# Kernel tuning notes

Measured on AMD Instinct MI355X. Metric: run time of the kernel, lower is better.

## Reference

```python
import jax, jax.numpy as jnp
import numpy as np

N_NODE = 8192
H1 = 512
R_EMB = 128
N_EDGE = 262144
N_REG = 2048


def gcn_conv(x, W, b, src, dst, n):
    """PyG-style GCNConv: add self-loops, sym-normalize, linear, scatter-add."""
    h = x @ W  # [n, out]
    loop = jnp.arange(n)
    src2 = jnp.concatenate([src, loop])
    dst2 = jnp.concatenate([dst, loop])
    ones = jnp.ones(src2.shape[0], dtype=h.dtype)
    deg = jax.ops.segment_sum(ones, dst2, num_segments=n)  # in-degree incl. self-loop
    dis = jnp.where(deg > 0, jax.lax.rsqrt(deg), 0.0)
    norm = dis[src2] * dis[dst2]  # [E+n]
    msg = h[src2] * norm[:, None]  # gather + scale
    return jax.ops.segment_sum(msg, dst2, num_segments=n) + b


def setup_inputs() -> dict:
    key = jax.random.key(0)
    k1, k2, k3, k4 = jax.random.split(key, 4)
    edge_index = jax.random.randint(k1, (N_EDGE, 2), 0, N_NODE)  # [E,2] (src,dst) pairs
    reg_id = jax.random.randint(k2, (N_REG,), 0, N_NODE)
    W1 = jax.random.normal(k3, (N_NODE, H1), dtype=jnp.float32) * 0.02
    b1 = jnp.zeros((H1,), dtype=jnp.float32)
    W2 = jax.random.normal(k4, (H1, R_EMB), dtype=jnp.float32) * 0.02
    b2 = jnp.zeros((R_EMB,), dtype=jnp.float32)
    return {"reg_id": reg_id, "edge_index": edge_index, "W1": W1, "b1": b1, "W2": W2, "b2": b2}


def reference(reg_id, edge_index, W1, b1, W2, b2):
    src = edge_index[:, 0]
    dst = edge_index[:, 1]
    n = W1.shape[0]
    x = jnp.eye(n, dtype=W1.dtype)  # identity feature matrix (one-hot per node)
    h = jax.nn.relu(gcn_conv(x, W1, b1, src, dst, n))
    # dropout is identity at inference
    out = gcn_conv(h, W2, b2, src, dst, n)  # [n, R_EMB]
    return out[reg_id]
```

## Files before the change

### kernel.cpp

```cpp
#include <hip/hip_runtime.h>
#include <hip/hip_bf16.h>

typedef unsigned int u32;

#define N_NODE 8192
#define H1 512
#define R_EMB 128
#define N_EDGE 262144
#define N_REG 2048

#define OFF_DEG        (0)
#define OFF_ROWSTART   (64 * 1024)
#define OFF_CURSOR     (128 * 1024)
#define OFF_DIS        (160 * 1024)
#define OFF_SORTED     (256 * 1024)
#define OFF_W1H        (2 * 1024 * 1024)
#define OFF_H1H        (10 * 1024 * 1024)
#define OFF_W2T        (18 * 1024 * 1024)
#define OFF_G          (19 * 1024 * 1024)

#define HALF_U32 (N_NODE * 128)

__device__ inline u32 rne_bf16(float f) {
    u32 u = __float_as_uint(f);
    u += 0x7fffu + ((u >> 16) & 1u);
    return u >> 16;
}
__device__ inline float bf_lo(u32 u) { return __uint_as_float(u << 16); }
__device__ inline float bf_hi(u32 u) { return __uint_as_float(u & 0xffff0000u); }

using frag_ab = __attribute__((ext_vector_type(8))) short;
using frag_cd = __attribute__((ext_vector_type(4))) float;

#define ACC4(v, q) \
    v##0 += bf_lo(q.x); v##1 += bf_hi(q.x); \
    v##2 += bf_lo(q.y); v##3 += bf_hi(q.y);

__global__ void hist_kernel(const int* __restrict__ edge, int* __restrict__ deg) {
    int e = blockIdx.x * blockDim.x + threadIdx.x;
    if (e < N_EDGE) {
        int dst = edge[2 * e + 1];
        atomicAdd(&deg[dst], 1);
    }
}

__global__ void scan_kernel(const int* __restrict__ deg, int* __restrict__ row_start,
                            int* __restrict__ cursor, float* __restrict__ dis) {
    __shared__ int wtot[16];
    __shared__ int wpre[16];
    int t = threadIdx.x;
    int lane = t & 63;
    int wv = t >> 6;
    int base = t * 8;
    int local[8];
    int sum = 0;
#pragma unroll
    for (int j = 0; j < 8; j++) {
        local[j] = deg[base + j];
        sum += local[j];
    }
    int sc = sum;
#pragma unroll
    for (int off = 1; off < 64; off <<= 1) {
        int y = __shfl_up(sc, off, 64);
        if (lane >= off) sc += y;
    }
    if (lane == 63) wtot[wv] = sc;
    __syncthreads();
    if (wv == 0 && lane < 16) {
        int v = wtot[lane];
        int s2 = v;
#pragma unroll
        for (int off = 1; off < 16; off <<= 1) {
            int y = __shfl_up(s2, off, 64);
            if (lane >= off) s2 += y;
        }
        wpre[lane] = s2 - v;
    }
    __syncthreads();
    int run = wpre[wv] + (sc - sum);
#pragma unroll
    for (int j = 0; j < 8; j++) {
        row_start[base + j] = run;
        cursor[base + j] = run;
        dis[base + j] = rsqrtf((float)(local[j] + 1));
        run += local[j];
    }
    if (t == 1023) row_start[N_NODE] = run;
}

__global__ void prep_kernel(const int* __restrict__ edge, int* __restrict__ cursor,
                            int* __restrict__ sorted_src,
                            const float* __restrict__ W1, const float* __restrict__ dis,
                            u32* __restrict__ W1h,
                            const float* __restrict__ W2, u32* __restrict__ w2t) {
    int bid = blockIdx.x;
    if (bid < 1024) {
        int e = bid * 256 + threadIdx.x;
        int src = edge[2 * e + 0];
        int dst = edge[2 * e + 1];
        int pos = atomicAdd(&cursor[dst], 1);
        sorted_src[pos] = src;
    } else if (bid < 5120) {
        int idx = (bid - 1024) * 256 + threadIdx.x;
        int j2 = idx & 63;
        int row = (idx >> 6) & 8191;
        int h = idx >> 19;
        float d = dis[row];
        float4 f = *(const float4*)(W1 + ((size_t)row << 9) + (h << 8) + (j2 << 2));
        uint2 o;
        o.x = rne_bf16(f.x * d) | (rne_bf16(f.y * d) << 16);
        o.y = rne_bf16(f.z * d) | (rne_bf16(f.w * d) << 16);
        *(uint2*)(W1h + ((size_t)h * HALF_U32) + (row << 7) + (j2 << 1)) = o;
    } else {
        int idx = (bid - 5120) * 256 + threadIdx.x;
        int j = idx >> 8;
        int p = idx & 255;
        float a = W2[(size_t)(2 * p) * R_EMB + j];
        float b = W2[(size_t)(2 * p + 1) * R_EMB + j];
        w2t[idx] = rne_bf16(a) | (rne_bf16(b) << 16);
    }
}

__global__ __launch_bounds__(256) void layer1_half(const u32* __restrict__ W1h,
                                                   const float* __restrict__ b1,
                                                   const int* __restrict__ row_start,
                                                   const int* __restrict__ sorted_src,
                                                   const float* __restrict__ dis,
                                                   u32* __restrict__ h1h) {
    int half = blockIdx.x >> 11;
    int d = ((blockIdx.x & 2047) << 2) + (threadIdx.x >> 6);
    int lane = threadIdx.x & 63;
    const u32* basep = W1h + (size_t)half * HALF_U32;
    int loff = lane << 1;
    float disd = dis[d];

    uint2 wd = *(const uint2*)(basep + (d << 7) + loff);
    float a0 = bf_lo(wd.x), a1 = bf_hi(wd.x), a2 = bf_lo(wd.y), a3 = bf_hi(wd.y);
    float c0 = 0, c1 = 0, c2 = 0, c3 = 0;

    int beg = row_start[d], end = row_start[d + 1];
    int i = beg;
    int rem = (end - beg) & 3;
    for (int r = 0; r < rem; r++) {
        int s = sorted_src[i++];
        uint2 v0 = *(const uint2*)(basep + (s << 7) + loff);
        ACC4(a, v0)
    }
    for (; i < end; i += 4) {
        int s0 = sorted_src[i];
        int s1 = sorted_src[i + 1];
        int s2 = sorted_src[i + 2];
        int s3 = sorted_src[i + 3];
        uint2 v0 = *(const uint2*)(basep + (s0 << 7) + loff);
        uint2 v1 = *(const uint2*)(basep + (s1 << 7) + loff);
        uint2 v2 = *(const uint2*)(basep + (s2 << 7) + loff);
        uint2 v3 = *(const uint2*)(basep + (s3 << 7) + loff);
        ACC4(a, v0)
        ACC4(c, v1)
        ACC4(a, v2)
        ACC4(c, v3)
    }
    a0 += c0; a1 += c1; a2 += c2; a3 += c3;

    float4 bb = *(const float4*)(b1 + (half << 8) + (lane << 2));
    float o0 = fmaxf(a0 * disd + bb.x, 0.0f) * disd;
    float o1 = fmaxf(a1 * disd + bb.y, 0.0f) * disd;
    float o2 = fmaxf(a2 * disd + bb.z, 0.0f) * disd;
    float o3 = fmaxf(a3 * disd + bb.w, 0.0f) * disd;
    uint2 o;
    o.x = rne_bf16(o0) | (rne_bf16(o1) << 16);
    o.y = rne_bf16(o2) | (rne_bf16(o3) << 16);
    *(uint2*)(h1h + (size_t)half * HALF_U32 + (d << 7) + loff) = o;
}

__global__ __launch_bounds__(256) void layer2_agg(const u32* __restrict__ h1h,
                                                  const int* __restrict__ reg_id,
                                                  const int* __restrict__ row_start,
                                                  const int* __restrict__ sorted_src,
                                                  const float* __restrict__ dis,
                                                  u32* __restrict__ g_bf) {
    int tgt = (blockIdx.x << 2) + (threadIdx.x >> 6);
    int lane = threadIdx.x & 63;
    int d = reg_id[tgt];
    int loff = lane << 1;
    float disd = dis[d];
    const u32* base0 = h1h;
    const u32* base1 = h1h + HALF_U32;

    uint2 wl = *(const uint2*)(base0 + (d << 7) + loff);
    uint2 wh = *(const uint2*)(base1 + (d << 7) + loff);
    float a0 = bf_lo(wl.x), a1 = bf_hi(wl.x), a2 = bf_lo(wl.y), a3 = bf_hi(wl.y);
    float a4 = bf_lo(wh.x), a5 = bf_hi(wh.x), a6 = bf_lo(wh.y), a7 = bf_hi(wh.y);
    float c0 = 0, c1 = 0, c2 = 0, c3 = 0, c4 = 0, c5 = 0, c6 = 0, c7 = 0;

    int beg = row_start[d], end = row_start[d + 1];
    int i = beg;
    if ((end - beg) & 1) {
        int s = sorted_src[i++];
        uint2 v0 = *(const uint2*)(base0 + (s << 7) + loff);
        uint2 v1 = *(const uint2*)(base1 + (s << 7) + loff);
        ACC4(a, v0)
        float t4 = bf_lo(v1.x), t5 = bf_hi(v1.x), t6 = bf_lo(v1.y), t7 = bf_hi(v1.y);
        a4 += t4; a5 += t5; a6 += t6; a7 += t7;
    }
    for (; i < end; i += 2) {
        int s0 = sorted_src[i];
        int s1 = sorted_src[i + 1];
        uint2 v0 = *(const uint2*)(base0 + (s0 << 7) + loff);
        uint2 v1 = *(const uint2*)(base1 + (s0 << 7) + loff);
        uint2 v2 = *(const uint2*)(base0 + (s1 << 7) + loff);
        uint2 v3 = *(const uint2*)(base1 + (s1 << 7) + loff);
        ACC4(a, v0)
        a4 += bf_lo(v1.x); a5 += bf_hi(v1.x); a6 += bf_lo(v1.y); a7 += bf_hi(v1.y);
        ACC4(c, v2)
        c4 += bf_lo(v3.x); c5 += bf_hi(v3.x); c6 += bf_lo(v3.y); c7 += bf_hi(v3.y);
    }
    a0 += c0; a1 += c1; a2 += c2; a3 += c3;
    a4 += c4; a5 += c5; a6 += c6; a7 += c7;

    uint2 ol, oh;
    ol.x = rne_bf16(a0 * disd) | (rne_bf16(a1 * disd) << 16);
    ol.y = rne_bf16(a2 * disd) | (rne_bf16(a3 * disd) << 16);
    oh.x = rne_bf16(a4 * disd) | (rne_bf16(a5 * disd) << 16);
    oh.y = rne_bf16(a6 * disd) | (rne_bf16(a7 * disd) << 16);
    u32* grow = g_bf + ((size_t)tgt << 8);
    *(uint2*)(grow + loff) = ol;
    *(uint2*)(grow + 128 + loff) = oh;
}

__global__ void gemm_out_mfma(const u32* __restrict__ g_bf, const u32* __restrict__ w2t_bf,
                              const float* __restrict__ b2, float* __restrict__ out) {
    int w = blockIdx.x * 4 + (threadIdx.x >> 6);
    int lane = threadIdx.x & 63;
    int tm = w >> 3;
    int tn = w & 7;
    int r15 = lane & 15;
    int kb4 = (lane >> 4) << 2;

    const uint4* arow = (const uint4*)(g_bf + ((tm * 16 + r15) << 8) + kb4);
    const uint4* brow = (const uint4*)(w2t_bf + ((tn * 16 + r15) << 8) + kb4);
    frag_cd acc = {0.0f, 0.0f, 0.0f, 0.0f};
#pragma unroll
    for (int kk = 0; kk < 16; kk++) {
        uint4 av = arow[kk * 4];
        uint4 bv = brow[kk * 4];
        acc = __builtin_amdgcn_mfma_f32_16x16x32_bf16(*(frag_ab*)&av, *(frag_ab*)&bv, acc, 0, 0, 0);
    }
    int col = tn * 16 + r15;
    int row0 = tm * 16 + ((lane >> 4) << 2);
    float bias = b2[col];
#pragma unroll
    for (int r = 0; r < 4; r++)
        out[(size_t)(row0 + r) * R_EMB + col] = acc[r] + bias;
}

extern "C" void kernel_launch(void* const* d_in, const int* in_sizes, int n_in,
                              void* d_out, int out_size, void* d_ws, size_t ws_size,
                              hipStream_t stream) {
    const int* reg_id = (const int*)d_in[0];
    const int* edge = (const int*)d_in[1];
    const float* W1 = (const float*)d_in[2];
    const float* b1 = (const float*)d_in[3];
    const float* W2 = (const float*)d_in[4];
    const float* b2 = (const float*)d_in[5];
    float* out = (float*)d_out;

    char* ws = (char*)d_ws;
    int* deg = (int*)(ws + OFF_DEG);
    int* row_start = (int*)(ws + OFF_ROWSTART);
    int* cursor = (int*)(ws + OFF_CURSOR);
    float* dis = (float*)(ws + OFF_DIS);
    int* sorted_src = (int*)(ws + OFF_SORTED);
    u32* W1h = (u32*)(ws + OFF_W1H);
    u32* h1h = (u32*)(ws + OFF_H1H);
    u32* w2t = (u32*)(ws + OFF_W2T);
    u32* g_bf = (u32*)(ws + OFF_G);

    hipMemsetAsync(deg, 0, N_NODE * sizeof(int), stream);

    hist_kernel<<<N_EDGE / 256, 256, 0, stream>>>(edge, deg);
    scan_kernel<<<1, 1024, 0, stream>>>(deg, row_start, cursor, dis);
    prep_kernel<<<5248, 256, 0, stream>>>(edge, cursor, sorted_src, W1, dis, W1h, W2, w2t);
    layer1_half<<<4096, 256, 0, stream>>>(W1h, b1, row_start, sorted_src, dis, h1h);
    layer2_agg<<<N_REG / 4, 256, 0, stream>>>(h1h, reg_id, row_start, sorted_src, dis, g_bf);
    gemm_out_mfma<<<256, 256, 0, stream>>>(g_bf, w2t, b2, out);
}
```

Baseline: 155.3 us.

## Apply layer-2 weight before aggregation to gather 128-wide rows instead of 512

Measured after the change: 162.2 us. 4.4% more time.

```diff
diff --git a/kernel.cpp b/kernel.cpp
--- a/kernel.cpp
+++ b/kernel.cpp
@@ -2,6 +2,7 @@
 #include <hip/hip_bf16.h>
 
 typedef unsigned int u32;
+typedef unsigned short u16;
 
 #define N_NODE 8192
 #define H1 512
@@ -15,9 +16,9 @@
 #define OFF_DIS        (160 * 1024)
 #define OFF_SORTED     (256 * 1024)
 #define OFF_W1H        (2 * 1024 * 1024)
-#define OFF_H1H        (10 * 1024 * 1024)
+#define OFF_H1S        (10 * 1024 * 1024)
 #define OFF_W2T        (18 * 1024 * 1024)
-#define OFF_G          (19 * 1024 * 1024)
+#define OFF_H2B        (19 * 1024 * 1024)
 
 #define HALF_U32 (N_NODE * 128)
 
@@ -122,14 +123,13 @@
     }
 }
 
-__global__ __launch_bounds__(256) void layer1_half(const u32* __restrict__ W1h,
-                                                   const float* __restrict__ b1,
-                                                   const int* __restrict__ row_start,
-                                                   const int* __restrict__ sorted_src,
-                                                   const float* __restrict__ dis,
-                                                   u32* __restrict__ h1h) {
-    int half = blockIdx.x >> 11;
-    int d = ((blockIdx.x & 2047) << 2) + (threadIdx.x >> 6);
+__global__ __launch_bounds__(256) void layer1_phase(const u32* __restrict__ W1h,
+                                                    const float* __restrict__ b1,
+                                                    const int* __restrict__ row_start,
+                                                    const int* __restrict__ sorted_src,
+                                                    const float* __restrict__ dis,
+                                                    u32* __restrict__ h1s, int half) {
+    int d = (blockIdx.x << 2) + (threadIdx.x >> 6);
     int lane = threadIdx.x & 63;
     const u32* basep = W1h + (size_t)half * HALF_U32;
     int loff = lane << 1;
@@ -171,66 +171,11 @@
     uint2 o;
     o.x = rne_bf16(o0) | (rne_bf16(o1) << 16);
     o.y = rne_bf16(o2) | (rne_bf16(o3) << 16);
-    *(uint2*)(h1h + (size_t)half * HALF_U32 + (d << 7) + loff) = o;
-}
-
-__global__ __launch_bounds__(256) void layer2_agg(const u32* __restrict__ h1h,
-                                                  const int* __restrict__ reg_id,
-                                                  const int* __restrict__ row_start,
-                                                  const int* __restrict__ sorted_src,
-                                                  const float* __restrict__ dis,
-                                                  u32* __restrict__ g_bf) {
-    int tgt = (blockIdx.x << 2) + (threadIdx.x >> 6);
-    int lane = threadIdx.x & 63;
-    int d = reg_id[tgt];
-    int loff = lane << 1;
-    float disd = dis[d];
-    const u32* base0 = h1h;
-    const u32* base1 = h1h + HALF_U32;
-
-    uint2 wl = *(const uint2*)(base0 + (d << 7) + loff);
-    uint2 wh = *(const uint2*)(base1 + (d << 7) + loff);
-    float a0 = bf_lo(wl.x), a1 = bf_hi(wl.x), a2 = bf_lo(wl.y), a3 = bf_hi(wl.y);
-    float a4 = bf_lo(wh.x), a5 = bf_hi(wh.x), a6 = bf_lo(wh.y), a7 = bf_hi(wh.y);
-    float c0 = 0, c1 = 0, c2 = 0, c3 = 0, c4 = 0, c5 = 0, c6 = 0, c7 = 0;
-
-    int beg = row_start[d], end = row_start[d + 1];
-    int i = beg;
-    if ((end - beg) & 1) {
-        int s = sorted_src[i++];
-        uint2 v0 = *(const uint2*)(base0 + (s << 7) + loff);
-        uint2 v1 = *(const uint2*)(base1 + (s << 7) + loff);
-        ACC4(a, v0)
-        float t4 = bf_lo(v1.x), t5 = bf_hi(v1.x), t6 = bf_lo(v1.y), t7 = bf_hi(v1.y);
-        a4 += t4; a5 += t5; a6 += t6; a7 += t7;
-    }
-    for (; i < end; i += 2) {
-        int s0 = sorted_src[i];
-        int s1 = sorted_src[i + 1];
-        uint2 v0 = *(const uint2*)(base0 + (s0 << 7) + loff);
-        uint2 v1 = *(const uint2*)(base1 + (s0 << 7) + loff);
-        uint2 v2 = *(const uint2*)(base0 + (s1 << 7) + loff);
-        uint2 v3 = *(const uint2*)(base1 + (s1 << 7) + loff);
-        ACC4(a, v0)
-        a4 += bf_lo(v1.x); a5 += bf_hi(v1.x); a6 += bf_lo(v1.y); a7 += bf_hi(v1.y);
-        ACC4(c, v2)
-        c4 += bf_lo(v3.x); c5 += bf_hi(v3.x); c6 += bf_lo(v3.y); c7 += bf_hi(v3.y);
-    }
-    a0 += c0; a1 += c1; a2 += c2; a3 += c3;
-    a4 += c4; a5 += c5; a6 += c6; a7 += c7;
-
-    uint2 ol, oh;
-    ol.x = rne_bf16(a0 * disd) | (rne_bf16(a1 * disd) << 16);
-    ol.y = rne_bf16(a2 * disd) | (rne_bf16(a3 * disd) << 16);
-    oh.x = rne_bf16(a4 * disd) | (rne_bf16(a5 * disd) << 16);
-    oh.y = rne_bf16(a6 * disd) | (rne_bf16(a7 * disd) << 16);
-    u32* grow = g_bf + ((size_t)tgt << 8);
-    *(uint2*)(grow + loff) = ol;
-    *(uint2*)(grow + 128 + loff) = oh;
-}
-
-__global__ void gemm_out_mfma(const u32* __restrict__ g_bf, const u32* __restrict__ w2t_bf,
-                              const float* __restrict__ b2, float* __restrict__ out) {
+    *(uint2*)(h1s + ((size_t)d << 8) + (half << 7) + loff) = o;
+}
+
+__global__ void gemm_h2(const u32* __restrict__ h1s, const u32* __restrict__ w2t_bf,
+                        u16* __restrict__ h2b) {
     int w = blockIdx.x * 4 + (threadIdx.x >> 6);
     int lane = threadIdx.x & 63;
     int tm = w >> 3;
@@ -238,7 +183,7 @@
     int r15 = lane & 15;
     int kb4 = (lane >> 4) << 2;
 
-    const uint4* arow = (const uint4*)(g_bf + ((tm * 16 + r15) << 8) + kb4);
+    const uint4* arow = (const uint4*)(h1s + ((tm * 16 + r15) << 8) + kb4);
     const uint4* brow = (const uint4*)(w2t_bf + ((tn * 16 + r15) << 8) + kb4);
     frag_cd acc = {0.0f, 0.0f, 0.0f, 0.0f};
 #pragma unroll
@@ -249,10 +194,56 @@
     }
     int col = tn * 16 + r15;
     int row0 = tm * 16 + ((lane >> 4) << 2);
-    float bias = b2[col];
 #pragma unroll
     for (int r = 0; r < 4; r++)
-        out[(size_t)(row0 + r) * R_EMB + col] = acc[r] + bias;
+        h2b[(size_t)(row0 + r) * R_EMB + col] = (u16)rne_bf16(acc[r]);
+}
+
+__global__ __launch_bounds__(256) void layer2_small(const u32* __restrict__ h2u,
+                                                    const int* __restrict__ reg_id,
+                                                    const int* __restrict__ row_start,
+                                                    const int* __restrict__ sorted_src,
+                                                    const float* __restrict__ dis,
+                                                    const float* __restrict__ b2,
+                                                    float* __restrict__ out) {
+    int tgt = (blockIdx.x << 2) + (threadIdx.x >> 6);
+    int lane = threadIdx.x & 63;
+    int d = reg_id[tgt];
+    float disd = dis[d];
+
+    u32 wd = h2u[(d << 6) + lane];
+    float a0 = bf_lo(wd), a1 = bf_hi(wd);
+    float c0 = 0, c1 = 0;
+
+    int beg = row_start[d], end = row_start[d + 1];
+    int i = beg;
+    int rem = (end - beg) & 3;
+    for (int r = 0; r < rem; r++) {
+        int s = sorted_src[i++];
+        u32 v = h2u[(s << 6) + lane];
+        a0 += bf_lo(v); a1 += bf_hi(v);
+    }
+    for (; i < end; i += 4) {
+        int s0 = sorted_src[i];
+        int s1 = sorted_src[i + 1];
+        int s2 = sorted_src[i + 2];
+        int s3 = sorted_src[i + 3];
+        u32 v0 = h2u[(s0 << 6) + lane];
+        u32 v1 = h2u[(s1 << 6) + lane];
+        u32 v2 = h2u[(s2 << 6) + lane];
+        u32 v3 = h2u[(s3 << 6) + lane];
+        a0 += bf_lo(v0); a1 += bf_hi(v0);
+        c0 += bf_lo(v1); c1 += bf_hi(v1);
+        a0 += bf_lo(v2); a1 += bf_hi(v2);
+        c0 += bf_lo(v3); c1 += bf_hi(v3);
+    }
+    a0 += c0; a1 += c1;
+
+    float2 bb = *(const float2*)(b2 + (lane << 1));
+    float2 o;
+    o.x = a0 * disd + bb.x;
+    o.y = a1 * disd + bb.y;
+    *(float2*)(out + ((size_t)tgt << 7) + (lane << 1)) = o;
 }
 
 extern "C" void kernel_launch(void* const* d_in, const int* in_sizes, int n_in,
@@ -273,16 +264,18 @@
     float* dis = (float*)(ws + OFF_DIS);
     int* sorted_src = (int*)(ws + OFF_SORTED);
     u32* W1h = (u32*)(ws + OFF_W1H);
-    u32* h1h = (u32*)(ws + OFF_H1H);
+    u32* h1s = (u32*)(ws + OFF_H1S);
     u32* w2t = (u32*)(ws + OFF_W2T);
-    u32* g_bf = (u32*)(ws + OFF_G);
+    u16* h2b = (u16*)(ws + OFF_H2B);
 
     hipMemsetAsync(deg, 0, N_NODE * sizeof(int), stream);
 
     hist_kernel<<<N_EDGE / 256, 256, 0, stream>>>(edge, deg);
     scan_kernel<<<1, 1024, 0, stream>>>(deg, row_start, cursor, dis);
     prep_kernel<<<5248, 256, 0, stream>>>(edge, cursor, sorted_src, W1, dis, W1h, W2, w2t);
-    layer1_half<<<4096, 256, 0, stream>>>(W1h, b1, row_start, sorted_src, dis, h1h);
-    layer2_agg<<<N_REG / 4, 256, 0, stream>>>(h1h, reg_id, row_start, sorted_src, dis, g_bf);
-    gemm_out_mfma<<<256, 256, 0, stream>>>(g_bf, w2t, b2, out);
-}
+    layer1_phase<<<2048, 256, 0, stream>>>(W1h, b1, row_start, sorted_src, dis, h1s, 0);
+    layer1_phase<<<2048, 256, 0, stream>>>(W1h, b1, row_start, sorted_src, dis, h1s, 1);
+    gemm_h2<<<1024, 256, 0, stream>>>(h1s, w2t, h2b);
+    layer2_small<<<N_REG / 4, 256, 0, stream>>>((const u32*)h2b, reg_id, row_start,
+                                                sorted_src, dis, b2, out);
+}
```
